# Kernel optimization log

Hardware: AMD Instinct MI355X
Metric: run time of the kernel (lower is better)

Reference implementation:

```python
import jax, jax.numpy as jnp
import numpy as np

B, S, D = 2, 2048, 1024
H, DH = 16, 64
N_CTX = 2048
IGNORE = -100000.0


def setup_inputs() -> dict:
    key = jax.random.key(0)
    ks = jax.random.split(key, 6)
    scale = 0.02
    return {
        "x": jax.random.normal(ks[0], (B, S, D), dtype=jnp.float32),
        "W_Q": jax.random.normal(ks[1], (H, DH, D), dtype=jnp.float32) * scale,
        "W_K": jax.random.normal(ks[2], (H, DH, D), dtype=jnp.float32) * scale,
        "W_V": jax.random.normal(ks[3], (H, DH, D), dtype=jnp.float32) * scale,
        "W_O": jax.random.normal(ks[4], (H, D, DH), dtype=jnp.float32) * scale,
        "b_Q": jnp.zeros((H, DH), dtype=jnp.float32),
        "b_K": jnp.zeros((H, DH), dtype=jnp.float32),
        "b_V": jnp.zeros((H, DH), dtype=jnp.float32),
        "b_O": jnp.zeros((D,), dtype=jnp.float32),
    }


def reference(x, W_Q, W_K, W_V, W_O, b_Q, b_K, b_V, b_O):
    attn_scale = jnp.sqrt(jnp.asarray(DH, dtype=x.dtype))
    # q,k,v: [batch, pos, head, d_head]
    q = jnp.einsum('ihm,bpm->bpih', W_Q, x) + b_Q
    k = jnp.einsum('ihm,bpm->bpih', W_K, x) + b_K
    v = jnp.einsum('ihm,bpm->bpih', W_V, x) + b_V
    # scores: [batch, head, q_pos, k_pos]
    attn_scores = jnp.einsum('bpih,bqih->bipq', q, k) / attn_scale
    # causal mask (pos_start=0, no kv cache)
    qs, ks_ = attn_scores.shape[-2], attn_scores.shape[-1]
    mask = jnp.tril(jnp.ones((qs, ks_), dtype=bool))
    attn_scores = jnp.where(mask, attn_scores, jnp.asarray(IGNORE, dtype=attn_scores.dtype))
    attn_matrix = jax.nn.softmax(attn_scores, axis=-1)
    # z: [batch, q_pos, head, d_head]
    z = jnp.einsum('bpih,biqp->bqih', v, attn_matrix)
    out = jnp.einsum('idh,bqih->bqd', W_O, z) + b_O
    return out
```

## Files before the change

### kernel.cpp

```cpp
#include <hip/hip_runtime.h>

typedef __bf16 bf16;
typedef __bf16 bf16x4 __attribute__((ext_vector_type(4)));
typedef __bf16 bf16x8 __attribute__((ext_vector_type(8)));
typedef float f32x4 __attribute__((ext_vector_type(4)));

#define AS1C(p) ((const __attribute__((address_space(1))) void*)(p))
#define AS3(p)  ((__attribute__((address_space(3))) void*)(p))

__device__ __forceinline__ void gld16(const bf16* gsrc, bf16* ldst) {
  __builtin_amdgcn_global_load_lds(AS1C(gsrc), AS3(ldst), 16, 0, 0);
}


__global__ void castx_kernel(const float* __restrict__ x, bf16* __restrict__ xb) {
  const int n4 = (4096 * 1024) / 4;
  for (int i = blockIdx.x * blockDim.x + threadIdx.x; i < n4; i += gridDim.x * blockDim.x) {
    float4 v = ((const float4*)x)[i];
    bf16x4 o;
    o[0] = (bf16)v.x; o[1] = (bf16)v.y; o[2] = (bf16)v.z; o[3] = (bf16)v.w;
    ((bf16x4*)xb)[i] = o;
  }
}

__global__ void prep_kernel(const float* __restrict__ WQ, const float* __restrict__ WK,
                            const float* __restrict__ WV, const float* __restrict__ WO,
                            const float* __restrict__ bQ, const float* __restrict__ bK,
                            const float* __restrict__ bV,
                            bf16* __restrict__ Wqkv, bf16* __restrict__ Wo2,
                            float* __restrict__ biasq) {
  const int WN = 1024 * 1024;
  const int total = 4 * WN + 3072;
  for (int i = blockIdx.x * blockDim.x + threadIdx.x; i < total; i += gridDim.x * blockDim.x) {
    if (i < WN) {
      Wqkv[i] = (bf16)(WQ[i] * 0.125f);
    } else if (i < 2 * WN) {
      Wqkv[i] = (bf16)WK[i - WN];
    } else if (i < 3 * WN) {
      Wqkv[i] = (bf16)WV[i - 2 * WN];
    } else if (i < 4 * WN) {
      int j = i - 3 * WN;
      int hh = j >> 16, r = j & 65535, d = r >> 6, dh = r & 63;
      Wo2[d * 1024 + hh * 64 + dh] = (bf16)WO[j];
    } else {
      int n = i - 4 * WN;
      biasq[n] = (n < 1024) ? bQ[n] * 0.125f : (n < 2048) ? bK[n - 1024] : bV[n - 2048];
    }
  }
}

template <int MODE>
__global__ __launch_bounds__(256)
void gemm_bt(const bf16* __restrict__ A, const bf16* __restrict__ Bw,
             const float* __restrict__ bias,
             bf16* __restrict__ Qo, bf16* __restrict__ Ko, bf16* __restrict__ Vt,
             float* __restrict__ Co, int M, int N, int K) {
  __shared__ bf16 As[128 * 64];
  __shared__ bf16 Bs[128 * 64];
  const int tid = threadIdx.x;
  const int lane = tid & 63, w = tid >> 6;
  const int wr = w >> 1, wc = w & 1;
  const int g = lane >> 4, lr = lane & 15;
  const int brow = blockIdx.x * 128, bcol = blockIdx.y * 128;

  f32x4 acc[4][4] = {};

  for (int k0 = 0; k0 < K; k0 += 64) {
#pragma unroll
    for (int it = 0; it < 4; ++it) {
      const int chunk = it * 4 + w;
      const int e = chunk * 64 + lane;
      const int row = e >> 3;
      const int c8 = (e & 7) << 3;
      gld16(A + (size_t)(brow + row) * K + k0 + c8, As + chunk * 512);
      gld16(Bw + (size_t)(bcol + row) * K + k0 + c8, Bs + chunk * 512);
    }
    __syncthreads();
#pragma unroll
    for (int kk = 0; kk < 2; ++kk) {
      bf16x8 af[4], bfm[4];
#pragma unroll
      for (int m = 0; m < 4; ++m)
        af[m] = *(const bf16x8*)(As + (wr * 64 + m * 16 + lr) * 64 + kk * 32 + g * 8);
#pragma unroll
      for (int n = 0; n < 4; ++n)
        bfm[n] = *(const bf16x8*)(Bs + (wc * 64 + n * 16 + lr) * 64 + kk * 32 + g * 8);
#pragma unroll
      for (int m = 0; m < 4; ++m)
#pragma unroll
        for (int n = 0; n < 4; ++n)
          acc[m][n] = __builtin_amdgcn_mfma_f32_16x16x32_bf16(af[m], bfm[n], acc[m][n], 0, 0, 0);
    }
    __syncthreads();
  }

  const int row0 = brow + wr * 64;
  const int col0 = bcol + wc * 64;
#pragma unroll
  for (int m = 0; m < 4; ++m) {
#pragma unroll
    for (int n = 0; n < 4; ++n) {
      const int nidx = col0 + n * 16 + lr;
      f32x4 v = acc[m][n];
      const float bs = bias[nidx];
      if (MODE == 0) {
        const int stream = nidx >> 10;
        const int j = nidx & 1023;
        const int hh = j >> 6, dh = j & 63;
        const int r0 = row0 + m * 16 + g * 4;
        const int b = r0 >> 11;
        const int p0 = r0 & 2047;
        if (stream == 2) {
          bf16x4 vv;
#pragma unroll
          for (int i = 0; i < 4; ++i) vv[i] = (bf16)(v[i] + bs);
          *(bf16x4*)(Vt + ((size_t)(b * 16 + hh) * 64 + dh) * 2048 + p0) = vv;
        } else {
          bf16* dst = (stream == 0) ? Qo : Ko;
#pragma unroll
          for (int i = 0; i < 4; ++i)
            dst[((size_t)(b * 16 + hh) * 2048 + (p0 + i)) * 64 + dh] = (bf16)(v[i] + bs);
        }
      } else {
#pragma unroll
        for (int i = 0; i < 4; ++i) {
          const int r = row0 + m * 16 + g * 4 + i;
          Co[(size_t)r * 1024 + nidx] = v[i] + bs;
        }
      }
    }
  }
}

__global__ __launch_bounds__(256, 2)
void attn_kernel(const bf16* __restrict__ Qm, const bf16* __restrict__ Km,
                 const bf16* __restrict__ Vm, bf16* __restrict__ Z) {
  const int pi = blockIdx.x, hh = blockIdx.y, b = blockIdx.z;
  const int bh = b * 16 + hh;
  const int lane = threadIdx.x & 63, w = threadIdx.x >> 6;
  const int g = lane >> 4, lr = lane & 15;
  __shared__ bf16 Ks[2][4096];
  __shared__ bf16 Vs[2][4096];
  __shared__ bf16 Plds[4][16][72];

  const bf16* Qb = Qm + (size_t)bh * 2048 * 64;
  const bf16* Kb = Km + (size_t)bh * 2048 * 64;
  const bf16* Vb = Vm + (size_t)bh * 64 * 2048;

  auto stage = [&](int kv0, int bufi) {
#pragma unroll
    for (int it = 0; it < 2; ++it) {
      const int cb = w * 128 + it * 64;
      const int u = cb + lane;
      const int lc = u ^ ((u >> 3) & 7);
      const int row = lc >> 3, c8 = (lc & 7) * 8;
      gld16(Kb + (size_t)(kv0 + row) * 64 + c8, &Ks[bufi][cb * 8]);
      gld16(Vb + (size_t)row * 2048 + kv0 + c8, &Vs[bufi][cb * 8]);
    }
  };

  for (int half = 0; half < 2; ++half) {
    const int qt = half ? 31 - pi : pi;
    const int q0 = qt * 64 + w * 16;

    bf16x8 aq[2];
#pragma unroll
    for (int kk = 0; kk < 2; ++kk)
      aq[kk] = *(const bf16x8*)(Qb + (size_t)(q0 + lr) * 64 + kk * 32 + g * 8);

    float m_i[4], l_i[4];
    f32x4 oacc[4] = {};
#pragma unroll
    for (int i = 0; i < 4; ++i) { m_i[i] = -1e30f; l_i[i] = 0.f; }

    stage(0, 0);
    __syncthreads();
    int buf = 0;

    for (int t = 0; t <= qt; ++t) {
      if (t < qt) stage((t + 1) * 64, buf ^ 1);

      f32x4 s[4] = {};
#pragma unroll
      for (int kk = 0; kk < 2; ++kk) {
#pragma unroll
        for (int n = 0; n < 4; ++n) {
          const int r = n * 16 + lr;
          const int slot = (r * 8 + kk * 4 + g) ^ (r & 7);
          bf16x8 bk = *(const bf16x8*)(&Ks[buf][slot * 8]);
          s[n] = __builtin_amdgcn_mfma_f32_16x16x32_bf16(aq[kk], bk, s[n], 0, 0, 0);
        }
      }
      if (t == qt) {
#pragma unroll
        for (int n = 0; n < 4; ++n) {
          const int key = n * 16 + lr;
#pragma unroll
          for (int i = 0; i < 4; ++i) {
            const int rr = w * 16 + g * 4 + i;
            if (key > rr) s[n][i] = -1e9f;
          }
        }
      }
      float tm[4], ts[4], al[4];
#pragma unroll
      for (int i = 0; i < 4; ++i)
        tm[i] = fmaxf(fmaxf(s[0][i], s[1][i]), fmaxf(s[2][i], s[3][i]));
#pragma unroll
      for (int d = 1; d < 16; d <<= 1)
#pragma unroll
        for (int i = 0; i < 4; ++i) tm[i] = fmaxf(tm[i], __shfl_xor(tm[i], d));
#pragma unroll
      for (int i = 0; i < 4; ++i) {
        const float mn = fmaxf(m_i[i], tm[i]);
        al[i] = __expf(m_i[i] - mn);
        m_i[i] = mn;
      }
      f32x4 p[4];
#pragma unroll
      for (int n = 0; n < 4; ++n)
#pragma unroll
        for (int i = 0; i < 4; ++i) p[n][i] = __expf(s[n][i] - m_i[i]);
#pragma unroll
      for (int i = 0; i < 4; ++i) ts[i] = p[0][i] + p[1][i] + p[2][i] + p[3][i];
#pragma unroll
      for (int d = 1; d < 16; d <<= 1)
#pragma unroll
        for (int i = 0; i < 4; ++i) ts[i] += __shfl_xor(ts[i], d);
#pragma unroll
      for (int i = 0; i < 4; ++i) l_i[i] = l_i[i] * al[i] + ts[i];
#pragma unroll
      for (int n = 0; n < 4; ++n)
#pragma unroll
        for (int i = 0; i < 4; ++i) oacc[n][i] *= al[i];
#pragma unroll
      for (int n = 0; n < 4; ++n)
#pragma unroll
        for (int i = 0; i < 4; ++i)
          Plds[w][g * 4 + i][n * 16 + lr] = (bf16)p[n][i];
#pragma unroll
      for (int kk = 0; kk < 2; ++kk) {
        bf16x8 pa = *(const bf16x8*)(&Plds[w][lr][kk * 32 + g * 8]);
#pragma unroll
        for (int n = 0; n < 4; ++n) {
          const int r = n * 16 + lr;
          const int slot = (r * 8 + kk * 4 + g) ^ (r & 7);
          bf16x8 bv = *(const bf16x8*)(&Vs[buf][slot * 8]);
          oacc[n] = __builtin_amdgcn_mfma_f32_16x16x32_bf16(pa, bv, oacc[n], 0, 0, 0);
        }
      }
      __syncthreads();
      buf ^= 1;
    }

#pragma unroll
    for (int i = 0; i < 4; ++i) l_i[i] = 1.f / l_i[i];
#pragma unroll
    for (int n = 0; n < 4; ++n)
#pragma unroll
      for (int i = 0; i < 4; ++i) {
        const int q = qt * 64 + w * 16 + g * 4 + i;
        Z[((size_t)(b * 2048 + q) * 16 + hh) * 64 + n * 16 + lr] = (bf16)(oacc[n][i] * l_i[i]);
      }
  }
}

extern "C" void kernel_launch(void* const* d_in, const int* in_sizes, int n_in,
                              void* d_out, int out_size, void* d_ws, size_t ws_size,
                              hipStream_t stream) {
  const float* x  = (const float*)d_in[0];
  const float* WQ = (const float*)d_in[1];
  const float* WK = (const float*)d_in[2];
  const float* WV = (const float*)d_in[3];
  const float* WO = (const float*)d_in[4];
  const float* bQ = (const float*)d_in[5];
  const float* bK = (const float*)d_in[6];
  const float* bV = (const float*)d_in[7];
  const float* bO = (const float*)d_in[8];
  float* out = (float*)d_out;

  char* ws = (char*)d_ws;
  bf16* xb    = (bf16*)(ws);
  bf16* Wqkv  = (bf16*)(ws + (8u << 20));
  bf16* Wo2   = (bf16*)(ws + (14u << 20));
  bf16* Qb    = (bf16*)(ws + (16u << 20));
  bf16* Kb    = (bf16*)(ws + (24u << 20));
  bf16* Vtb   = (bf16*)(ws + (32u << 20));
  bf16* Zb    = (bf16*)(ws + (40u << 20));
  float* biasq = (float*)(ws + (48u << 20));

  castx_kernel<<<2048, 256, 0, stream>>>(x, xb);
  prep_kernel<<<2048, 256, 0, stream>>>(WQ, WK, WV, WO, bQ, bK, bV, Wqkv, Wo2, biasq);
  gemm_bt<0><<<dim3(32, 24), 256, 0, stream>>>(xb, Wqkv, biasq, Qb, Kb, Vtb, nullptr,
                                               4096, 3072, 1024);
  attn_kernel<<<dim3(16, 16, 2), 256, 0, stream>>>(Qb, Kb, Vtb, Zb);
  gemm_bt<1><<<dim3(32, 8), 256, 0, stream>>>(Zb, Wo2, bO, nullptr, nullptr, nullptr, out,
                                              4096, 1024, 1024);
}
```

Baseline: 232.0 us.

## Transpose attention MFMA layout, shuffle P in registers, remap grid per XCD

The attention kernel now computes S^T (K as the A operand), so each lane owns a single query row. That reduces softmax reductions to two cross-group shuffles. P is repacked into MFMA B-operand layout with register shuffles instead of an LDS round trip, which removes the Plds buffer. The causal half-pairing is dropped in favour of one q-tile per block, with a 1D grid of 1024 blocks remapped so each XCD handles whole heads for L2 locality, and launch bounds are raised to 4 blocks per CU. Having one tile per block risks load imbalance from causal work skew, and Z writes become vectorised bf16x4 stores.

```diff
diff --git a/kernel.cpp b/kernel.cpp
--- a/kernel.cpp
+++ b/kernel.cpp
@@ -4,6 +4,7 @@
 typedef __bf16 bf16x4 __attribute__((ext_vector_type(4)));
 typedef __bf16 bf16x8 __attribute__((ext_vector_type(8)));
 typedef float f32x4 __attribute__((ext_vector_type(4)));
+typedef unsigned u32x4 __attribute__((ext_vector_type(4)));
 
 #define AS1C(p) ((const __attribute__((address_space(1))) void*)(p))
 #define AS3(p)  ((__attribute__((address_space(3))) void*)(p))
@@ -132,16 +133,21 @@
   }
 }
 
-__global__ __launch_bounds__(256, 2)
+__global__ __launch_bounds__(256, 4)
 void attn_kernel(const bf16* __restrict__ Qm, const bf16* __restrict__ Km,
                  const bf16* __restrict__ Vm, bf16* __restrict__ Z) {
-  const int pi = blockIdx.x, hh = blockIdx.y, b = blockIdx.z;
+  const int nblk = blockIdx.x;
+  const int xcd = nblk & 7, slot = nblk >> 3;
+  const int G = ((slot >> 5) << 3) + xcd;
+  const int qt = slot & 31;
+  const int hh = G & 15, b = G >> 4;
   const int bh = b * 16 + hh;
   const int lane = threadIdx.x & 63, w = threadIdx.x >> 6;
   const int g = lane >> 4, lr = lane & 15;
+  const bool g0 = g & 1, g1 = (g >> 1) & 1;
+
   __shared__ bf16 Ks[2][4096];
   __shared__ bf16 Vs[2][4096];
-  __shared__ bf16 Plds[4][16][72];
 
   const bf16* Qb = Qm + (size_t)bh * 2048 * 64;
   const bf16* Kb = Km + (size_t)bh * 2048 * 64;
@@ -159,109 +165,129 @@
     }
   };
 
-  for (int half = 0; half < 2; ++half) {
-    const int qt = half ? 31 - pi : pi;
-    const int q0 = qt * 64 + w * 16;
-
-    bf16x8 aq[2];
-#pragma unroll
-    for (int kk = 0; kk < 2; ++kk)
-      aq[kk] = *(const bf16x8*)(Qb + (size_t)(q0 + lr) * 64 + kk * 32 + g * 8);
-
-    float m_i[4], l_i[4];
-    f32x4 oacc[4] = {};
-#pragma unroll
-    for (int i = 0; i < 4; ++i) { m_i[i] = -1e30f; l_i[i] = 0.f; }
-
-    stage(0, 0);
+  const int q0w = qt * 64 + w * 16;
+  const int qg = q0w + lr;
+
+  bf16x8 aq[2];
+#pragma unroll
+  for (int kk = 0; kk < 2; ++kk)
+    aq[kk] = *(const bf16x8*)(Qb + (size_t)qg * 64 + kk * 32 + g * 8);
+
+  float m_i = -1e30f, l_i = 0.f;
+  f32x4 oacc[4] = {};
+
+  stage(0, 0);
+  __syncthreads();
+  int buf = 0;
+
+  for (int t = 0; t <= qt; ++t) {
+    if (t < qt) stage((t + 1) * 64, buf ^ 1);
+    const int kv0 = t * 64;
+
+    f32x4 s[4] = {};
+#pragma unroll
+    for (int kk = 0; kk < 2; ++kk) {
+#pragma unroll
+      for (int n = 0; n < 4; ++n) {
+        const int r = n * 16 + lr;
+        const int sl = (r * 8 + kk * 4 + g) ^ (r & 7);
+        bf16x8 bk = *(const bf16x8*)(&Ks[buf][sl * 8]);
+        s[n] = __builtin_amdgcn_mfma_f32_16x16x32_bf16(bk, aq[kk], s[n], 0, 0, 0);
+      }
+    }
+    if (t == qt) {
+#pragma unroll
+      for (int n = 0; n < 4; ++n)
+#pragma unroll
+        for (int i = 0; i < 4; ++i)
+          if (kv0 + n * 16 + g * 4 + i > qg) s[n][i] = -1e9f;
+    }
+
+    float tm = fmaxf(fmaxf(fmaxf(s[0][0], s[0][1]), fmaxf(s[0][2], s[0][3])),
+                     fmaxf(fmaxf(s[1][0], s[1][1]), fmaxf(s[1][2], s[1][3])));
+    tm = fmaxf(tm, fmaxf(fmaxf(fmaxf(s[2][0], s[2][1]), fmaxf(s[2][2], s[2][3])),
+                         fmaxf(fmaxf(s[3][0], s[3][1]), fmaxf(s[3][2], s[3][3]))));
+    tm = fmaxf(tm, __shfl_xor(tm, 16));
+    tm = fmaxf(tm, __shfl_xor(tm, 32));
+    const float mn = fmaxf(m_i, tm);
+    const float al = __expf(m_i - mn);
+    m_i = mn;
+#pragma unroll
+    for (int n = 0; n < 4; ++n)
+#pragma unroll
+      for (int i = 0; i < 4; ++i) s[n][i] = __expf(s[n][i] - mn);
+    float ts = ((s[0][0] + s[0][1]) + (s[0][2] + s[0][3])) +
+               ((s[1][0] + s[1][1]) + (s[1][2] + s[1][3])) +
+               ((s[2][0] + s[2][1]) + (s[2][2] + s[2][3])) +
+               ((s[3][0] + s[3][1]) + (s[3][2] + s[3][3]));
+    ts += __shfl_xor(ts, 16);
+    ts += __shfl_xor(ts, 32);
+    l_i = l_i * al + ts;
+#pragma unroll
+    for (int n = 0; n < 4; ++n)
+#pragma unroll
+      for (int i = 0; i < 4; ++i) oacc[n][i] *= al;
+
+    unsigned U[8];
+#pragma unroll
+    for (int n = 0; n < 4; ++n)
+#pragma unroll
+      for (int h = 0; h < 2; ++h) {
+        unsigned lo = (unsigned)__builtin_bit_cast(unsigned short, (bf16)s[n][2 * h]);
+        unsigned hi = (unsigned)__builtin_bit_cast(unsigned short, (bf16)s[n][2 * h + 1]);
+        U[n * 2 + h] = lo | (hi << 16);
+      }
+    unsigned rA0 = (unsigned)__shfl_xor((int)(g1 ? U[0] : U[2]), 32);
+    unsigned rA1 = (unsigned)__shfl_xor((int)(g1 ? U[1] : U[3]), 32);
+    unsigned rA2 = (unsigned)__shfl_xor((int)(g1 ? U[4] : U[6]), 32);
+    unsigned rA3 = (unsigned)__shfl_xor((int)(g1 ? U[5] : U[7]), 32);
+    unsigned v2_000 = g1 ? rA0 : U[0];
+    unsigned v2_001 = g1 ? rA1 : U[1];
+    unsigned v2_010 = g1 ? U[2] : rA0;
+    unsigned v2_011 = g1 ? U[3] : rA1;
+    unsigned v2_100 = g1 ? rA2 : U[4];
+    unsigned v2_101 = g1 ? rA3 : U[5];
+    unsigned v2_110 = g1 ? U[6] : rA2;
+    unsigned v2_111 = g1 ? U[7] : rA3;
+    unsigned rB0 = (unsigned)__shfl_xor((int)(g0 ? v2_000 : v2_010), 16);
+    unsigned rB1 = (unsigned)__shfl_xor((int)(g0 ? v2_001 : v2_011), 16);
+    unsigned rB2 = (unsigned)__shfl_xor((int)(g0 ? v2_100 : v2_110), 16);
+    unsigned rB3 = (unsigned)__shfl_xor((int)(g0 ? v2_101 : v2_111), 16);
+    u32x4 t0, t1;
+    t0[0] = g0 ? rB0 : v2_000;
+    t0[1] = g0 ? rB1 : v2_001;
+    t0[2] = g0 ? v2_010 : rB0;
+    t0[3] = g0 ? v2_011 : rB1;
+    t1[0] = g0 ? rB2 : v2_100;
+    t1[1] = g0 ? rB3 : v2_101;
+    t1[2] = g0 ? v2_110 : rB2;
+    t1[3] = g0 ? v2_111 : rB3;
+    bf16x8 pb0 = __builtin_bit_cast(bf16x8, t0);
+    bf16x8 pb1 = __builtin_bit_cast(bf16x8, t1);
+
+#pragma unroll
+    for (int kk = 0; kk < 2; ++kk) {
+      const bf16x8 pb = kk ? pb1 : pb0;
+#pragma unroll
+      for (int n = 0; n < 4; ++n) {
+        const int r = n * 16 + lr;
+        const int sl = (r * 8 + kk * 4 + g) ^ (r & 7);
+        bf16x8 av = *(const bf16x8*)(&Vs[buf][sl * 8]);
+        oacc[n] = __builtin_amdgcn_mfma_f32_16x16x32_bf16(av, pb, oacc[n], 0, 0, 0);
+      }
+    }
     __syncthreads();
-    int buf = 0;
-
-    for (int t = 0; t <= qt; ++t) {
-      if (t < qt) stage((t + 1) * 64, buf ^ 1);
-
-      f32x4 s[4] = {};
-#pragma unroll
-      for (int kk = 0; kk < 2; ++kk) {
-#pragma unroll
-        for (int n = 0; n < 4; ++n) {
-          const int r = n * 16 + lr;
-          const int slot = (r * 8 + kk * 4 + g) ^ (r & 7);
-          bf16x8 bk = *(const bf16x8*)(&Ks[buf][slot * 8]);
-          s[n] = __builtin_amdgcn_mfma_f32_16x16x32_bf16(aq[kk], bk, s[n], 0, 0, 0);
-        }
-      }
-      if (t == qt) {
-#pragma unroll
-        for (int n = 0; n < 4; ++n) {
-          const int key = n * 16 + lr;
-#pragma unroll
-          for (int i = 0; i < 4; ++i) {
-            const int rr = w * 16 + g * 4 + i;
-            if (key > rr) s[n][i] = -1e9f;
-          }
-        }
-      }
-      float tm[4], ts[4], al[4];
-#pragma unroll
-      for (int i = 0; i < 4; ++i)
-        tm[i] = fmaxf(fmaxf(s[0][i], s[1][i]), fmaxf(s[2][i], s[3][i]));
-#pragma unroll
-      for (int d = 1; d < 16; d <<= 1)
-#pragma unroll
-        for (int i = 0; i < 4; ++i) tm[i] = fmaxf(tm[i], __shfl_xor(tm[i], d));
-#pragma unroll
-      for (int i = 0; i < 4; ++i) {
-        const float mn = fmaxf(m_i[i], tm[i]);
-        al[i] = __expf(m_i[i] - mn);
-        m_i[i] = mn;
-      }
-      f32x4 p[4];
-#pragma unroll
-      for (int n = 0; n < 4; ++n)
-#pragma unroll
-        for (int i = 0; i < 4; ++i) p[n][i] = __expf(s[n][i] - m_i[i]);
-#pragma unroll
-      for (int i = 0; i < 4; ++i) ts[i] = p[0][i] + p[1][i] + p[2][i] + p[3][i];
-#pragma unroll
-      for (int d = 1; d < 16; d <<= 1)
-#pragma unroll
-        for (int i = 0; i < 4; ++i) ts[i] += __shfl_xor(ts[i], d);
-#pragma unroll
-      for (int i = 0; i < 4; ++i) l_i[i] = l_i[i] * al[i] + ts[i];
-#pragma unroll
-      for (int n = 0; n < 4; ++n)
-#pragma unroll
-        for (int i = 0; i < 4; ++i) oacc[n][i] *= al[i];
-#pragma unroll
-      for (int n = 0; n < 4; ++n)
-#pragma unroll
-        for (int i = 0; i < 4; ++i)
-          Plds[w][g * 4 + i][n * 16 + lr] = (bf16)p[n][i];
-#pragma unroll
-      for (int kk = 0; kk < 2; ++kk) {
-        bf16x8 pa = *(const bf16x8*)(&Plds[w][lr][kk * 32 + g * 8]);
-#pragma unroll
-        for (int n = 0; n < 4; ++n) {
-          const int r = n * 16 + lr;
-          const int slot = (r * 8 + kk * 4 + g) ^ (r & 7);
-          bf16x8 bv = *(const bf16x8*)(&Vs[buf][slot * 8]);
-          oacc[n] = __builtin_amdgcn_mfma_f32_16x16x32_bf16(pa, bv, oacc[n], 0, 0, 0);
-        }
-      }
-      __syncthreads();
-      buf ^= 1;
-    }
-
-#pragma unroll
-    for (int i = 0; i < 4; ++i) l_i[i] = 1.f / l_i[i];
-#pragma unroll
-    for (int n = 0; n < 4; ++n)
-#pragma unroll
-      for (int i = 0; i < 4; ++i) {
-        const int q = qt * 64 + w * 16 + g * 4 + i;
-        Z[((size_t)(b * 2048 + q) * 16 + hh) * 64 + n * 16 + lr] = (bf16)(oacc[n][i] * l_i[i]);
-      }
+    buf ^= 1;
+  }
+
+  const float li = 1.f / l_i;
+  bf16* zrow = Z + ((size_t)(b * 2048 + qg) * 16 + hh) * 64;
+#pragma unroll
+  for (int n = 0; n < 4; ++n) {
+    bf16x4 o4;
+#pragma unroll
+    for (int i = 0; i < 4; ++i) o4[i] = (bf16)(oacc[n][i] * li);
+    *(bf16x4*)(zrow + n * 16 + g * 4) = o4;
   }
 }
 
@@ -293,7 +319,7 @@
   prep_kernel<<<2048, 256, 0, stream>>>(WQ, WK, WV, WO, bQ, bK, bV, Wqkv, Wo2, biasq);
   gemm_bt<0><<<dim3(32, 24), 256, 0, stream>>>(xb, Wqkv, biasq, Qb, Kb, Vtb, nullptr,
                                                4096, 3072, 1024);
-  attn_kernel<<<dim3(16, 16, 2), 256, 0, stream>>>(Qb, Kb, Vtb, Zb);
+  attn_kernel<<<1024, 256, 0, stream>>>(Qb, Kb, Vtb, Zb);
   gemm_bt<1><<<dim3(32, 8), 256, 0, stream>>>(Zb, Wo2, bO, nullptr, nullptr, nullptr, out,
                                               4096, 1024, 1024);
 }
```

Result: slower. 243.9 us (+5.1%).
